# Optimization experiments

Measured on AMD Instinct MI355X. Metric: run time of the kernel, lower is better.

Reference implementation:

```python
import jax, jax.numpy as jnp
import numpy as np

B, T, F = 4096, 60, 64
H = 128          # num_hidden[0] == num_hidden[1]
FC1_IN, FC1_OUT = T * H, 512   # 7680 -> 512
LEN_OUT = 60


def setup_inputs() -> dict:
    key = jax.random.key(0)
    ks = jax.random.split(key, 14)
    s1 = 1.0 / np.sqrt(H)
    def u(k, shape, s):
        return jax.random.uniform(k, shape, jnp.float32, -s, s)
    return {
        "X_cont": jax.random.normal(ks[0], (B, T, F), jnp.float32),
        # LSTM layer 1 (PyTorch gate order i,f,g,o)
        "W_ih1": u(ks[1], (4 * H, F), s1),
        "W_hh1": u(ks[2], (4 * H, H), s1),
        "b_ih1": u(ks[3], (4 * H,), s1),
        "b_hh1": u(ks[4], (4 * H,), s1),
        # LSTM layer 2
        "W_ih2": u(ks[5], (4 * H, H), s1),
        "W_hh2": u(ks[6], (4 * H, H), s1),
        "b_ih2": u(ks[7], (4 * H,), s1),
        "b_hh2": u(ks[8], (4 * H,), s1),
        # FC head
        "W_fc1": u(ks[9], (FC1_OUT, FC1_IN), 1.0 / np.sqrt(FC1_IN)),
        "b_fc1": u(ks[10], (FC1_OUT,), 1.0 / np.sqrt(FC1_IN)),
        "W_fc2": u(ks[11], (LEN_OUT, FC1_OUT), 1.0 / np.sqrt(FC1_OUT)),
        "b_fc2": u(ks[12], (LEN_OUT,), 1.0 / np.sqrt(FC1_OUT)),
    }


def _lstm_layer(x, W_ih, W_hh, b_ih, b_hh):
    # x: [B,T,Fin]; zero initial (h,c); returns full hidden sequence [B,T,H]
    b, h = x.shape[0], W_hh.shape[1]
    # precompute input contribution for all timesteps (one big GEMM)
    xg = jnp.einsum('btf,gf->btg', x, W_ih) + b_ih + b_hh  # [B,T,4H]

    def step(carry, xt):
        hp, cp = carry
        g = xt + hp @ W_hh.T                                # [B,4H]
        i, f, gg, o = jnp.split(g, 4, axis=-1)
        i = jax.nn.sigmoid(i)
        f = jax.nn.sigmoid(f)
        gg = jnp.tanh(gg)
        o = jax.nn.sigmoid(o)
        c = f * cp + i * gg
        hn = o * jnp.tanh(c)
        return (hn, c), hn

    h0 = jnp.zeros((b, h), x.dtype)
    _, hs = jax.lax.scan(step, (h0, h0), jnp.swapaxes(xg, 0, 1))  # [T,B,H]
    return jnp.swapaxes(hs, 0, 1)


def reference(X_cont, W_ih1, W_hh1, b_ih1, b_hh1,
              W_ih2, W_hh2, b_ih2, b_hh2,
              W_fc1, b_fc1, W_fc2, b_fc2):
    b = X_cont.shape[0]
    h1 = _lstm_layer(X_cont, W_ih1, W_hh1, b_ih1, b_hh1)   # [B,T,H]
    h2 = _lstm_layer(h1, W_ih2, W_hh2, b_ih2, b_hh2)       # [B,T,H]
    flat = h2.reshape(b, -1)                               # [B, T*H] = [B,7680]
    fc1 = flat @ W_fc1.T + b_fc1                           # [B,512]
    fc2 = fc1 @ W_fc2.T + b_fc2                            # [B,length_out]
    return fc2.reshape(b, LEN_OUT, 1)
```

## Files before the change

kernel.cpp:

```cpp
#include <hip/hip_runtime.h>
#include <hip/hip_fp16.h>
#include <cstdint>

typedef _Float16 h16;
typedef _Float16 half8 __attribute__((ext_vector_type(8)));
typedef float floatx4 __attribute__((ext_vector_type(4)));

#define T_SZ 60
#define H_SZ 128
#define NB_FC1 7680

#define LOG2E  1.44269504088896340736f
#define LOG2E2 2.88539008177792681472f

__device__ __forceinline__ float sigm(float x) {
    float e = __builtin_amdgcn_exp2f(x * -LOG2E);
    return __builtin_amdgcn_rcpf(1.0f + e);
}
__device__ __forceinline__ float tanh_fast(float x) {
    float e = __builtin_amdgcn_exp2f(x * LOG2E2);
    return 1.0f - 2.0f * __builtin_amdgcn_rcpf(e + 1.0f);
}

template<int INDIM, bool IN_F32>
__global__ __launch_bounds__(512, 1)
void lstm_layer(const void* __restrict__ in_v,
                const float* __restrict__ W_ih,
                const float* __restrict__ W_hh,
                const float* __restrict__ b_ih,
                const float* __restrict__ b_hh,
                h16* __restrict__ h_out)
{
    constexpr int KT_IN = INDIM / 32;
    __shared__ __align__(16) h16 hist[16][16][H_SZ];

    const int tid  = threadIdx.x;
    const int w    = tid >> 6;
    const int lane = tid & 63;
    const int lrow = lane & 15;
    const int lgrp = lane >> 4;
    const size_t base_row = (size_t)blockIdx.x * 16;

    half8 wf_in[4][KT_IN];
    half8 wf_hh[4][4];
    float bias[4];

    #pragma unroll
    for (int q = 0; q < 4; ++q) {
        const int n = (w + 8 * q) * 16 + lrow;
        bias[q] = b_ih[n] + b_hh[n];
        #pragma unroll
        for (int kt = 0; kt < KT_IN; ++kt) {
            const float* p = W_ih + (size_t)n * INDIM + kt * 32 + lgrp * 8;
            half8 v;
            #pragma unroll
            for (int j = 0; j < 8; ++j) v[j] = (h16)p[j];
            wf_in[q][kt] = v;
        }
        #pragma unroll
        for (int kt = 0; kt < 4; ++kt) {
            const float* p = W_hh + (size_t)n * H_SZ + kt * 32 + lgrp * 8;
            half8 v;
            #pragma unroll
            for (int j = 0; j < 8; ++j) v[j] = (h16)p[j];
            wf_hh[q][kt] = v;
        }
    }

    const float* inF = (const float*)in_v;
    const h16*   inH = (const h16*)in_v;

    floatx4 raw[KT_IN][2];
    half8   xs[KT_IN];

    auto load_x = [&](int t) {
        #pragma unroll
        for (int kt = 0; kt < KT_IN; ++kt) {
            if constexpr (IN_F32) {
                const float* p = inF + ((base_row + lrow) * T_SZ + t) * INDIM + kt * 32 + lgrp * 8;
                raw[kt][0] = *(const floatx4*)(p);
                raw[kt][1] = *(const floatx4*)(p + 4);
            } else {
                xs[kt] = *(const half8*)(inH + ((base_row + lrow) * T_SZ + t) * INDIM + kt * 32 + lgrp * 8);
            }
        }
    };

    auto get_x = [&](half8 (&xf)[KT_IN]) {
        #pragma unroll
        for (int kt = 0; kt < KT_IN; ++kt) {
            if constexpr (IN_F32) {
                const auto p0 = __builtin_amdgcn_cvt_pkrtz(raw[kt][0][0], raw[kt][0][1]);
                const auto p1 = __builtin_amdgcn_cvt_pkrtz(raw[kt][0][2], raw[kt][0][3]);
                const auto p2 = __builtin_amdgcn_cvt_pkrtz(raw[kt][1][0], raw[kt][1][1]);
                const auto p3 = __builtin_amdgcn_cvt_pkrtz(raw[kt][1][2], raw[kt][1][3]);
                half8 v;
                v[0] = (h16)p0[0]; v[1] = (h16)p0[1]; v[2] = (h16)p1[0]; v[3] = (h16)p1[1];
                v[4] = (h16)p2[0]; v[5] = (h16)p2[1]; v[6] = (h16)p3[0]; v[7] = (h16)p3[1];
                xf[kt] = v;
            } else {
                xf[kt] = xs[kt];
            }
        }
    };

    floatx4 c4 = {0.f, 0.f, 0.f, 0.f};
    const int colW = 16 * w + lrow;

    auto flush = [&](int t) {
        half8 vals[4];
        int   time[4], row[4], cg[4];
        #pragma unroll
        for (int s = 0; s < 4; ++s) {
            const int u = tid + 512 * s;
            time[s] = t - 7 + (u >> 8);
            row[s]  = (u >> 4) & 15;
            cg[s]   = u & 15;
            vals[s] = *(const half8*)&hist[time[s] & 15][row[s]][(cg[s] * 8) ^ ((row[s] & 7) << 3)];
        }
        #pragma unroll
        for (int s = 0; s < 4; ++s)
            *(half8*)(h_out + ((base_row + row[s]) * T_SZ + time[s]) * H_SZ + cg[s] * 8) = vals[s];
    };

    floatx4 accA[4], accB[4];
    load_x(0);
    {
        half8 xf[KT_IN];
        get_x(xf);
        #pragma unroll
        for (int q = 0; q < 4; ++q) accA[q] = floatx4{bias[q], bias[q], bias[q], bias[q]};
        #pragma unroll
        for (int kt = 0; kt < KT_IN; ++kt)
            #pragma unroll
            for (int q = 0; q < 4; ++q)
                accA[q] = __builtin_amdgcn_mfma_f32_16x16x32_f16(xf[kt], wf_in[q][kt], accA[q], 0, 0, 0);
        load_x(1);
    }

    auto step = [&](int t, floatx4 (&accC)[4], floatx4 (&accN)[4]) {
        half8 hf[4];
        const bool have_h = (t > 0);
        if (have_h) {
            const h16* hb = &hist[(t - 1) & 15][0][0];
            #pragma unroll
            for (int kt = 0; kt < 4; ++kt) {
                const int col0 = kt * 32 + lgrp * 8;
                hf[kt] = *(const half8*)(hb + lrow * H_SZ + (col0 ^ ((lrow & 7) << 3)));
            }
        }

        if (t + 1 < T_SZ) {
            half8 xf[KT_IN];
            get_x(xf);
            #pragma unroll
            for (int q = 0; q < 4; ++q) accN[q] = floatx4{bias[q], bias[q], bias[q], bias[q]};
            #pragma unroll
            for (int kt = 0; kt < KT_IN; ++kt)
                #pragma unroll
                for (int q = 0; q < 4; ++q)
                    accN[q] = __builtin_amdgcn_mfma_f32_16x16x32_f16(xf[kt], wf_in[q][kt], accN[q], 0, 0, 0);
            if (t + 2 < T_SZ) load_x(t + 2);
        }

        if (have_h) {
            #pragma unroll
            for (int kt = 0; kt < 4; ++kt)
                #pragma unroll
                for (int q = 0; q < 4; ++q)
                    accC[q] = __builtin_amdgcn_mfma_f32_16x16x32_f16(hf[kt], wf_hh[q][kt], accC[q], 0, 0, 0);
        }

        h16 hcast[4];
        #pragma unroll
        for (int r = 0; r < 4; ++r) {
            const float gi = sigm(accC[0][r]);
            const float gf = sigm(accC[1][r]);
            const float gg = tanh_fast(accC[2][r]);
            const float go = sigm(accC[3][r]);
            const float cc = gf * c4[r] + gi * gg;
            c4[r] = cc;
            hcast[r] = (h16)(go * tanh_fast(cc));
        }
        h16* hb2 = &hist[t & 15][0][0];
        #pragma unroll
        for (int r = 0; r < 4; ++r) {
            const int rowW = lgrp * 4 + r;
            hb2[rowW * H_SZ + (colW ^ ((rowW & 7) << 3))] = hcast[r];
        }

        asm volatile("s_waitcnt lgkmcnt(0)" ::: "memory");
        __builtin_amdgcn_s_barrier();
        asm volatile("" ::: "memory");

        if (((t & 7) == 7) || (t == T_SZ - 1)) flush(t);
    };

    #pragma unroll 1
    for (int tt = 0; tt < T_SZ; tt += 2) {
        step(tt,     accA, accB);
        step(tt + 1, accB, accA);
    }
}

__global__ __launch_bounds__(256, 2)
void wc_kernel(const float* __restrict__ W_fc1,
               const float* __restrict__ W_fc2,
               h16* __restrict__ Wc)
{
    const int tid  = threadIdx.x;
    const int wv   = tid >> 6;
    const int lane = tid & 63;
    const int lrow = lane & 15;
    const int lgrp = lane >> 4;
    const int j0   = blockIdx.x * 64 + wv * 16;

    floatx4 acc[4];
    #pragma unroll
    for (int mt = 0; mt < 4; ++mt) acc[mt] = floatx4{0.f, 0.f, 0.f, 0.f};

    for (int kt = 0; kt < 16; ++kt) {
        const int k0 = kt * 32 + lgrp * 8;
        half8 bf;
        #pragma unroll
        for (int i = 0; i < 8; ++i)
            bf[i] = (h16)W_fc1[(size_t)(k0 + i) * NB_FC1 + j0 + lrow];
        #pragma unroll
        for (int mt = 0; mt < 4; ++mt) {
            const int m = mt * 16 + lrow;
            half8 af = {};
            if (m < 60) {
                const float* p = W_fc2 + (size_t)m * 512 + k0;
                const floatx4 f0 = *(const floatx4*)(p);
                const floatx4 f1 = *(const floatx4*)(p + 4);
                const auto p0 = __builtin_amdgcn_cvt_pkrtz(f0[0], f0[1]);
                const auto p1 = __builtin_amdgcn_cvt_pkrtz(f0[2], f0[3]);
                const auto p2 = __builtin_amdgcn_cvt_pkrtz(f1[0], f1[1]);
                const auto p3 = __builtin_amdgcn_cvt_pkrtz(f1[2], f1[3]);
                af[0] = (h16)p0[0]; af[1] = (h16)p0[1]; af[2] = (h16)p1[0]; af[3] = (h16)p1[1];
                af[4] = (h16)p2[0]; af[5] = (h16)p2[1]; af[6] = (h16)p3[0]; af[7] = (h16)p3[1];
            }
            acc[mt] = __builtin_amdgcn_mfma_f32_16x16x32_f16(af, bf, acc[mt], 0, 0, 0);
        }
    }

    #pragma unroll
    for (int mt = 0; mt < 4; ++mt)
        #pragma unroll
        for (int r = 0; r < 4; ++r) {
            const int m = mt * 16 + lgrp * 4 + r;
            if (m < 60) Wc[(size_t)m * NB_FC1 + j0 + lrow] = (h16)acc[mt][r];
        }
}

__global__ void bc_kernel(const float* __restrict__ W_fc2, const float* __restrict__ b_fc1,
                          const float* __restrict__ b_fc2, float* __restrict__ bc)
{
    const int m = blockIdx.x, t = threadIdx.x;
    float p = W_fc2[m * 512 + t] * b_fc1[t] + W_fc2[m * 512 + 256 + t] * b_fc1[256 + t];
    #pragma unroll
    for (int off = 1; off < 64; off <<= 1) p += __shfl_xor(p, off);
    __shared__ float sred[4];
    if ((t & 63) == 0) sred[t >> 6] = p;
    __syncthreads();
    if (t == 0) bc[m] = sred[0] + sred[1] + sred[2] + sred[3] + b_fc2[m];
}

__global__ __launch_bounds__(256, 2)
void fc_kernel(const h16* __restrict__ h2,
               const h16* __restrict__ Wc,
               const float* __restrict__ bcv,
               float* __restrict__ out)
{
    __shared__ float red[4][4][16][16];
    const int tid = threadIdx.x;
    const int w = tid >> 6, lane = tid & 63, lrow = lane & 15, lgrp = lane >> 4;
    const size_t base_row = (size_t)blockIdx.x * 16;

    floatx4 acc[4];
    #pragma unroll
    for (int q = 0; q < 4; ++q) acc[q] = floatx4{0.f, 0.f, 0.f, 0.f};

    const h16* arow = h2 + (base_row + lrow) * NB_FC1;
    for (int i = 0; i < 60; ++i) {
        const int kt = w * 60 + i;
        const int k0 = kt * 32 + lgrp * 8;
        const half8 a = *(const half8*)(arow + k0);
        #pragma unroll
        for (int q = 0; q < 4; ++q) {
            const int n = q * 16 + lrow;
            half8 b = 0;
            if (n < 60) b = *(const half8*)(Wc + (size_t)n * NB_FC1 + k0);
            acc[q] = __builtin_amdgcn_mfma_f32_16x16x32_f16(a, b, acc[q], 0, 0, 0);
        }
    }
    #pragma unroll
    for (int q = 0; q < 4; ++q)
        #pragma unroll
        for (int r = 0; r < 4; ++r)
            red[w][q][lgrp * 4 + r][lrow] = acc[q][r];
    __syncthreads();

    #pragma unroll
    for (int s = 0; s < 4; ++s) {
        const int idx = tid + 256 * s;
        const int row = idx >> 6, col = idx & 63;
        if (col < 60) {
            const int q = col >> 4, cin = col & 15;
            const float v = red[0][q][row][cin] + red[1][q][row][cin]
                          + red[2][q][row][cin] + red[3][q][row][cin];
            out[(base_row + row) * 60 + col] = v + bcv[col];
        }
    }
}

extern "C" void kernel_launch(void* const* d_in, const int* in_sizes, int n_in,
                              void* d_out, int out_size, void* d_ws, size_t ws_size,
                              hipStream_t stream)
{
    const float* X      = (const float*)d_in[0];
    const float* W_ih1  = (const float*)d_in[1];
    const float* W_hh1  = (const float*)d_in[2];
    const float* b_ih1  = (const float*)d_in[3];
    const float* b_hh1  = (const float*)d_in[4];
    const float* W_ih2  = (const float*)d_in[5];
    const float* W_hh2  = (const float*)d_in[6];
    const float* b_ih2  = (const float*)d_in[7];
    const float* b_hh2  = (const float*)d_in[8];
    const float* W_fc1  = (const float*)d_in[9];
    const float* b_fc1  = (const float*)d_in[10];
    const float* W_fc2  = (const float*)d_in[11];
    const float* b_fc2  = (const float*)d_in[12];

    h16* h1 = (h16*)d_ws;
    h16* h2 = h1 + (size_t)4096 * NB_FC1;
    h16* Wc = h2 + (size_t)4096 * NB_FC1;
    float* bc = (float*)(Wc + (size_t)60 * NB_FC1);

    wc_kernel<<<120, 256, 0, stream>>>(W_fc1, W_fc2, Wc);
    bc_kernel<<<60, 256, 0, stream>>>(W_fc2, b_fc1, b_fc2, bc);
    lstm_layer<64,  true ><<<256, 512, 0, stream>>>((const void*)X,  W_ih1, W_hh1, b_ih1, b_hh1, h1);
    lstm_layer<128, false><<<256, 512, 0, stream>>>((const void*)h1, W_ih2, W_hh2, b_ih2, b_hh2, h2);
    fc_kernel<<<256, 256, 0, stream>>>(h2, Wc, bc, (float*)d_out);
}
```

Before: 238.8 us.

## Fuse FC head into second LSTM layer, consuming hidden history from LDS

The second LSTM layer now accumulates the collapsed FC product directly from its shared-memory hidden-state history every 8 steps, then reduces across waves and writes the final output. This drops the separate fc_kernel launch and the fp16 write and read of the full h2 sequence through global memory. In exchange, the recurrent kernel does extra MFMA work and Wc loads at flush points on its critical serial path. It also holds more registers and a larger LDS reduction buffer at the end.

```diff
diff --git a/kernel.cpp b/kernel.cpp
--- a/kernel.cpp
+++ b/kernel.cpp
@@ -22,14 +22,17 @@
     return 1.0f - 2.0f * __builtin_amdgcn_rcpf(e + 1.0f);
 }
 
-template<int INDIM, bool IN_F32>
+template<int INDIM, bool IN_F32, bool FUSE_FC>
 __global__ __launch_bounds__(512, 1)
 void lstm_layer(const void* __restrict__ in_v,
                 const float* __restrict__ W_ih,
                 const float* __restrict__ W_hh,
                 const float* __restrict__ b_ih,
                 const float* __restrict__ b_hh,
-                h16* __restrict__ h_out)
+                h16* __restrict__ h_out,
+                const h16* __restrict__ Wc,
+                const float* __restrict__ bcv,
+                float* __restrict__ out)
 {
     constexpr int KT_IN = INDIM / 32;
     __shared__ __align__(16) h16 hist[16][16][H_SZ];
@@ -107,6 +110,10 @@
     floatx4 c4 = {0.f, 0.f, 0.f, 0.f};
     const int colW = 16 * w + lrow;
 
+    floatx4 acc_fc[4];
+    #pragma unroll
+    for (int q = 0; q < 4; ++q) acc_fc[q] = floatx4{0.f, 0.f, 0.f, 0.f};
+
     auto flush = [&](int t) {
         half8 vals[4];
         int   time[4], row[4], cg[4];
@@ -121,6 +128,22 @@
         #pragma unroll
         for (int s = 0; s < 4; ++s)
             *(half8*)(h_out + ((base_row + row[s]) * T_SZ + time[s]) * H_SZ + cg[s] * 8) = vals[s];
+    };
+
+    auto fc_acc = [&](int wstart, int nI) {
+        const int d0 = (w & 3) * 32 + lgrp * 8;
+        for (int i = 0; i < nI; ++i) {
+            const int t_abs = wstart + (w >> 2) + 2 * i;
+            const half8 af = *(const half8*)&hist[t_abs & 15][lrow][d0 ^ ((lrow & 7) << 3)];
+            const size_t kflat = (size_t)t_abs * H_SZ + (w & 3) * 32 + lgrp * 8;
+            #pragma unroll
+            for (int q = 0; q < 4; ++q) {
+                const int n = q * 16 + lrow;
+                half8 bf = {};
+                if (n < 60) bf = *(const half8*)(Wc + (size_t)n * NB_FC1 + kflat);
+                acc_fc[q] = __builtin_amdgcn_mfma_f32_16x16x32_f16(af, bf, acc_fc[q], 0, 0, 0);
+            }
+        }
     };
 
     floatx4 accA[4], accB[4];
@@ -193,13 +216,40 @@
         __builtin_amdgcn_s_barrier();
         asm volatile("" ::: "memory");
 
-        if (((t & 7) == 7) || (t == T_SZ - 1)) flush(t);
+        if constexpr (FUSE_FC) {
+            if ((t & 7) == 7)        fc_acc(t - 7, 4);
+            else if (t == T_SZ - 1)  fc_acc(56, 2);
+        } else {
+            if (((t & 7) == 7) || (t == T_SZ - 1)) flush(t);
+        }
     };
 
     #pragma unroll 1
     for (int tt = 0; tt < T_SZ; tt += 2) {
         step(tt,     accA, accB);
         step(tt + 1, accB, accA);
+    }
+
+    if constexpr (FUSE_FC) {
+        __shared__ float red[8][4][16][16];
+        #pragma unroll
+        for (int q = 0; q < 4; ++q)
+            #pragma unroll
+            for (int r = 0; r < 4; ++r)
+                red[w][q][lgrp * 4 + r][lrow] = acc_fc[q][r];
+        __syncthreads();
+        #pragma unroll
+        for (int s = 0; s < 2; ++s) {
+            const int idx = tid + 512 * s;
+            const int row = idx >> 6, col = idx & 63;
+            if (col < 60) {
+                const int q = col >> 4, cin = col & 15;
+                float v = 0.f;
+                #pragma unroll
+                for (int ww = 0; ww < 8; ++ww) v += red[ww][q][row][cin];
+                out[(base_row + row) * 60 + col] = v + bcv[col];
+            }
+        }
     }
 }
 
@@ -264,54 +314,6 @@
     if ((t & 63) == 0) sred[t >> 6] = p;
     __syncthreads();
     if (t == 0) bc[m] = sred[0] + sred[1] + sred[2] + sred[3] + b_fc2[m];
-}
-
-__global__ __launch_bounds__(256, 2)
-void fc_kernel(const h16* __restrict__ h2,
-               const h16* __restrict__ Wc,
-               const float* __restrict__ bcv,
-               float* __restrict__ out)
-{
-    __shared__ float red[4][4][16][16];
-    const int tid = threadIdx.x;
-    const int w = tid >> 6, lane = tid & 63, lrow = lane & 15, lgrp = lane >> 4;
-    const size_t base_row = (size_t)blockIdx.x * 16;
-
-    floatx4 acc[4];
-    #pragma unroll
-    for (int q = 0; q < 4; ++q) acc[q] = floatx4{0.f, 0.f, 0.f, 0.f};
-
-    const h16* arow = h2 + (base_row + lrow) * NB_FC1;
-    for (int i = 0; i < 60; ++i) {
-        const int kt = w * 60 + i;
-        const int k0 = kt * 32 + lgrp * 8;
-        const half8 a = *(const half8*)(arow + k0);
-        #pragma unroll
-        for (int q = 0; q < 4; ++q) {
-            const int n = q * 16 + lrow;
-            half8 b = 0;
-            if (n < 60) b = *(const half8*)(Wc + (size_t)n * NB_FC1 + k0);
-            acc[q] = __builtin_amdgcn_mfma_f32_16x16x32_f16(a, b, acc[q], 0, 0, 0);
-        }
-    }
-    #pragma unroll
-    for (int q = 0; q < 4; ++q)
-        #pragma unroll
-        for (int r = 0; r < 4; ++r)
-            red[w][q][lgrp * 4 + r][lrow] = acc[q][r];
-    __syncthreads();
-
-    #pragma unroll
-    for (int s = 0; s < 4; ++s) {
-        const int idx = tid + 256 * s;
-        const int row = idx >> 6, col = idx & 63;
-        if (col < 60) {
-            const int q = col >> 4, cin = col & 15;
-            const float v = red[0][q][row][cin] + red[1][q][row][cin]
-                          + red[2][q][row][cin] + red[3][q][row][cin];
-            out[(base_row + row) * 60 + col] = v + bcv[col];
-        }
-    }
 }
 
 extern "C" void kernel_launch(void* const* d_in, const int* in_sizes, int n_in,
@@ -333,13 +335,13 @@
     const float* b_fc2  = (const float*)d_in[12];
 
     h16* h1 = (h16*)d_ws;
-    h16* h2 = h1 + (size_t)4096 * NB_FC1;
-    h16* Wc = h2 + (size_t)4096 * NB_FC1;
+    h16* Wc = h1 + (size_t)4096 * NB_FC1;
     float* bc = (float*)(Wc + (size_t)60 * NB_FC1);
 
     wc_kernel<<<120, 256, 0, stream>>>(W_fc1, W_fc2, Wc);
     bc_kernel<<<60, 256, 0, stream>>>(W_fc2, b_fc1, b_fc2, bc);
-    lstm_layer<64,  true ><<<256, 512, 0, stream>>>((const void*)X,  W_ih1, W_hh1, b_ih1, b_hh1, h1);
-    lstm_layer<128, false><<<256, 512, 0, stream>>>((const void*)h1, W_ih2, W_hh2, b_ih2, b_hh2, h2);
-    fc_kernel<<<256, 256, 0, stream>>>(h2, Wc, bc, (float*)d_out);
-}
+    lstm_layer<64,  true,  false><<<256, 512, 0, stream>>>(
+        (const void*)X,  W_ih1, W_hh1, b_ih1, b_hh1, h1, nullptr, nullptr, nullptr);
+    lstm_layer<128, false, true ><<<256, 512, 0, stream>>>(
+        (const void*)h1, W_ih2, W_hh2, b_ih2, b_hh2, nullptr, Wc, bc, (float*)d_out);
+}
```

Measured after the change: 315.6 us. 32.1% more time.
